# Optimization experiments

Measured on AMD Instinct MI355X. Metric: run time of the kernel, lower is better.

The kernel has to match this reference:

```python
import jax, jax.numpy as jnp
import numpy as np

B, N, E, V, D, H = 16, 4096, 524288, 4, 64, 128
MLP_IN = H + 3 + 2  # node feats + conditioning coords + two temperature scalars
SRC_T, TGT_T = 300.0, 600.0
SCALE_RANGE = 0.5


def _w(k, shape):
    return (jax.random.normal(k, shape, jnp.float32) / np.sqrt(shape[0])).astype(jnp.float32)


def setup_inputs() -> dict:
    key = jax.random.key(0)
    ks = jax.random.split(key, 32)
    inp = {
        "coordinates": jax.random.normal(ks[0], (B, N, 3), jnp.float32),
        "atom_types": jax.random.randint(ks[1], (B, N), 0, V, jnp.int32),
        "adj_list": jax.random.randint(ks[2], (E, 2), 0, N, jnp.int32),
        "edge_batch_idx": jax.random.randint(ks[3], (E,), 0, B, jnp.int32),
        "masked_elements": jnp.zeros((B, N), bool),
        # message-passing GNN params
        "embed": jax.random.normal(ks[4], (V, D), jnp.float32),
        "W_in": _w(ks[5], (D + 3, H)), "b_in": jnp.zeros(H, jnp.float32),
        "W_msg0": _w(ks[6], (2 * H, H)), "b_msg0": jnp.zeros(H, jnp.float32),
        "W_upd0": _w(ks[7], (2 * H, H)), "b_upd0": jnp.zeros(H, jnp.float32),
        "W_msg1": _w(ks[8], (2 * H, H)), "b_msg1": jnp.zeros(H, jnp.float32),
        "W_upd1": _w(ks[9], (2 * H, H)), "b_upd1": jnp.zeros(H, jnp.float32),
        "W_out": _w(ks[10], (H, H)), "b_out": jnp.zeros(H, jnp.float32),
        # scale MLP (random small weights instead of zero init so output is non-trivial)
        "Ws0": _w(ks[11], (MLP_IN, H)), "bs0": jnp.zeros(H, jnp.float32),
        "Ws1": _w(ks[12], (H, H)), "bs1": jnp.zeros(H, jnp.float32),
        "Ws2": _w(ks[13], (H, H // 2)), "bs2": jnp.zeros(H // 2, jnp.float32),
        "Ws3": _w(ks[14], (H // 2, 3)) * 0.1, "bs3": jnp.zeros(3, jnp.float32),
        # shift MLP
        "Wt0": _w(ks[15], (MLP_IN, H)), "bt0": jnp.zeros(H, jnp.float32),
        "Wt1": _w(ks[16], (H, H)), "bt1": jnp.zeros(H, jnp.float32),
        "Wt2": _w(ks[17], (H, H // 2)), "bt2": jnp.zeros(H // 2, jnp.float32),
        "Wt3": _w(ks[18], (H // 2, 3)) * 0.1, "bt3": jnp.zeros(3, jnp.float32),
    }
    return inp


def _mlp(x, layers):
    for Wl, bl in layers[:-1]:
        x = jax.nn.relu(x @ Wl + bl)
    Wl, bl = layers[-1]
    return x @ Wl + bl


def reference(coordinates, atom_types, adj_list, edge_batch_idx, masked_elements,
              embed, W_in, b_in, W_msg0, b_msg0, W_upd0, b_upd0,
              W_msg1, b_msg1, W_upd1, b_upd1, W_out, b_out,
              Ws0, bs0, Ws1, bs1, Ws2, bs2, Ws3, bs3,
              Wt0, bt0, Wt1, bt1, Wt2, bt2, Wt3, bt3):
    Bn, Nn, _ = coordinates.shape
    valid = ~masked_elements                              # [B,N]
    vf = valid[..., None].astype(coordinates.dtype)
    # ---- message passing GNN ----
    h = jnp.concatenate([embed[atom_types], coordinates], -1)  # [B,N,D+3]
    h = jax.nn.relu(h @ W_in + b_in) * vf
    hf = h.reshape(Bn * Nn, -1)
    src = edge_batch_idx * Nn + adj_list[:, 0]
    dst = edge_batch_idx * Nn + adj_list[:, 1]
    for Wm, bm, Wu, bu in ((W_msg0, b_msg0, W_upd0, b_upd0),
                           (W_msg1, b_msg1, W_upd1, b_upd1)):
        m = jax.nn.relu(jnp.concatenate([hf[src], hf[dst]], -1) @ Wm + bm)  # [E,H]
        agg = jax.ops.segment_sum(m, dst, num_segments=Bn * Nn)             # [B*N,H]
        hf = jax.nn.relu(jnp.concatenate([hf, agg], -1) @ Wu + bu)
    node_feats = (hf @ W_out + b_out).reshape(Bn, Nn, -1) * vf              # [B,N,H]
    # ---- coupling transform (phase=0: atoms with type>0 are transformed) ----
    coupling = (atom_types > 0) & valid                  # [B,N]
    cond = coordinates * (~coupling)[..., None].astype(coordinates.dtype)
    temps = jnp.broadcast_to(jnp.asarray([SRC_T, TGT_T], coordinates.dtype), (Bn, Nn, 2))
    x = jnp.concatenate([node_feats, cond, temps], -1)   # [B,N,H+5]
    raw_scales = _mlp(x, [(Ws0, bs0), (Ws1, bs1), (Ws2, bs2), (Ws3, bs3)])
    shifts = _mlp(x, [(Wt0, bt0), (Wt1, bt1), (Wt2, bt2), (Wt3, bt3)])
    m3 = coupling[..., None].astype(coordinates.dtype)   # [B,N,1]
    log_scales = jnp.tanh(raw_scales) * SCALE_RANGE * m3 * vf
    shifts = shifts * m3
    log_det = log_scales.sum((1, 2))                     # [B]
    out = jnp.exp(log_scales) * coordinates + shifts
    out = jnp.where(coupling[..., None], out, coordinates)
    return out, log_det
```

## Files before the change

kernel.cpp:

```cpp
#include <hip/hip_runtime.h>

#define NB    16
#define NN    4096
#define NNODE (NB*NN)
#define NE    524288

typedef __attribute__((ext_vector_type(8))) short bf16x8_t;
typedef __attribute__((ext_vector_type(4))) float f32x4_t;

__device__ __forceinline__ unsigned short f2bf(float f) {
    union { float f; unsigned u; } v; v.f = f;
    return (unsigned short)((v.u + 0x7FFFu + ((v.u >> 16) & 1u)) >> 16);
}
__device__ __forceinline__ float bf2f(unsigned short h) {
    union { unsigned u; float f; } v; v.u = ((unsigned)h) << 16;
    return v.f;
}

__device__ __forceinline__ void gld16(const void* g, void* l) {
    __builtin_amdgcn_global_load_lds(
        (const __attribute__((address_space(1))) unsigned int*)g,
        (__attribute__((address_space(3))) unsigned int*)l, 16, 0, 0);
}

__global__ void deg_k(const int* __restrict__ adj, const int* __restrict__ ebi, int* __restrict__ deg)
{
    int e = blockIdx.x * 256 + threadIdx.x;
    atomicAdd(&deg[ebi[e] * NN + adj[2 * e + 1]], 1);
}

__global__ void scan_k(const int* __restrict__ deg, int* __restrict__ offs)
{
    __shared__ int sums[1024];
    int t = threadIdx.x;
    int base = t * 64;
    int s = 0;
    for (int i = 0; i < 64; ++i) s += deg[base + i];
    sums[t] = s;
    __syncthreads();
    for (int off = 1; off < 1024; off <<= 1) {
        int add = (t >= off) ? sums[t - off] : 0;
        __syncthreads();
        sums[t] += add;
        __syncthreads();
    }
    int run = (t > 0) ? sums[t - 1] : 0;
    for (int i = 0; i < 64; ++i) { offs[base + i] = run; run += deg[base + i]; }
    if (t == 1023) offs[NNODE] = run;
}

__global__ void scat_k(const int* __restrict__ adj, const int* __restrict__ ebi,
                       const int* __restrict__ offs, int* __restrict__ cur, int* __restrict__ esrc)
{
    int e = blockIdx.x * 256 + threadIdx.x;
    int bb = ebi[e];
    int d = bb * NN + adj[2 * e + 1];
    int s = bb * NN + adj[2 * e + 0];
    esrc[offs[d] + atomicAdd(&cur[d], 1)] = s;
}

__global__ void prep_k(const float* __restrict__ Wm0, const float* __restrict__ Wm1,
                       const float* __restrict__ Wu0, const float* __restrict__ Wu1,
                       const float* __restrict__ Wout,
                       const float* __restrict__ Ws0, const float* __restrict__ Wt0,
                       const float* __restrict__ Ws1, const float* __restrict__ Wt1,
                       const float* __restrict__ Ws2, const float* __restrict__ Wt2,
                       const float* __restrict__ bs0, const float* __restrict__ bt0,
                       const float* __restrict__ bs1, const float* __restrict__ bt1,
                       const float* __restrict__ bs2, const float* __restrict__ bt2,
                       const float* __restrict__ bm0, const float* __restrict__ bm1,
                       unsigned short* __restrict__ Btm0, unsigned short* __restrict__ Btm1,
                       unsigned short* __restrict__ Btu0, unsigned short* __restrict__ Btu1,
                       unsigned short* __restrict__ WoutP,
                       unsigned short* __restrict__ Bt0cat, unsigned short* __restrict__ Bt1cat,
                       unsigned short* __restrict__ Bt2cat,
                       float* __restrict__ b0cat, float* __restrict__ b1cat,
                       float* __restrict__ b2cat,
                       float* __restrict__ bm0cat, float* __restrict__ bm1cat)
{
    int bid = blockIdx.x, tx = threadIdx.x;
    if (bid < 256) {
        const float* W = bid < 128 ? Wm0 : Wm1;
        unsigned short* Bt = bid < 128 ? Btm0 : Btm1;
        int idx = (bid & 127) * 256 + tx;
        int n = idx >> 7, k = idx & 127;
        float v = (n < 128) ? W[k * 128 + n] : W[(128 + k) * 128 + (n - 128)];
        Bt[n * 128 + k] = f2bf(v);
    } else if (bid < 512) {
        const float* W = bid < 384 ? Wu0 : Wu1;
        unsigned short* Bt = bid < 384 ? Btu0 : Btu1;
        int idx = ((bid - 256) & 127) * 256 + tx;
        int n = idx >> 8, k = idx & 255;
        Bt[n * 256 + k] = f2bf(W[k * 128 + n]);
    } else if (bid < 576) {
        int idx = (bid - 512) * 256 + tx;
        int n = idx >> 7, k = idx & 127;
        WoutP[n * 128 + k] = f2bf(Wout[k * 128 + n]);
    } else if (bid < 768) {
        int idx = (bid - 576) * 256 + tx;
        int n = idx / 192, kk = idx % 192;
        const float* W = n < 128 ? Ws0 : Wt0;
        int nn = n & 127;
        Bt0cat[n * 192 + kk] = f2bf(kk < 133 ? W[kk * 128 + nn] : 0.f);
    } else if (bid < 896) {
        int idx = (bid - 768) * 256 + tx;
        int n = idx >> 7, k = idx & 127;
        const float* W = n < 128 ? Ws1 : Wt1;
        Bt1cat[n * 128 + k] = f2bf(W[k * 128 + (n & 127)]);
    } else if (bid < 1024) {
        int idx = (bid - 896) * 256 + tx;
        int n = idx >> 7, k = idx & 127;
        const float* W = n < 128 ? Ws2 : Wt2;
        int nn = n & 127;
        Bt2cat[n * 128 + k] = f2bf(nn < 64 ? W[k * 64 + nn] : 0.f);
    } else if (bid == 1024) {
        b0cat[tx] = (tx < 128) ? bs0[tx] : bt0[tx - 128];
    } else if (bid == 1025) {
        b1cat[tx] = (tx < 128) ? bs1[tx] : bt1[tx - 128];
    } else if (bid == 1026) {
        int nn = tx & 127;
        b2cat[tx] = (nn < 64) ? ((tx < 128) ? bs2[nn] : bt2[nn]) : 0.f;
    } else if (bid == 1027) {
        bm0cat[tx] = (tx < 128) ? 0.f : bm0[tx - 128];
    } else {
        bm1cat[tx] = (tx < 128) ? 0.f : bm1[tx - 128];
    }
}

__device__ __forceinline__ void msg_phase(const char* act, char* Bs,
    const unsigned short* __restrict__ Bt, const float* __restrict__ bias,
    unsigned short* __restrict__ P12, size_t row0, int tx)
{
    const int wid = tx >> 6, l = tx & 63;
    const int wr = wid >> 1, wc = wid & 1;
    const int rsel = l & 15, kq = l >> 4;
    const int rg = l >> 4, cc = l & 15;
#pragma unroll
    for (int nh = 0; nh < 2; ++nh) {
        f32x4_t acc[2][4];
#pragma unroll
        for (int i = 0; i < 2; ++i)
#pragma unroll
            for (int j = 0; j < 4; ++j) { f32x4_t z = {0.f,0.f,0.f,0.f}; acc[i][j] = z; }
#pragma unroll
        for (int kc = 0; kc < 128; kc += 64) {
            __syncthreads();
#pragma unroll
            for (int p = 0; p < 4; ++p) {
                int idx = tx + p * 256;
                int n = idx >> 3, kg = idx & 7;
                int kgs = kg ^ (n & 7);
                gld16(Bt + (size_t)(nh * 128 + n) * 128 + kc + kgs * 8, Bs + idx * 16);
            }
            __syncthreads();
#pragma unroll
            for (int ks = 0; ks < 2; ++ks) {
                bf16x8_t af[2], bv[4];
#pragma unroll
                for (int fm = 0; fm < 2; ++fm) {
                    int r = wr * 32 + fm * 16 + rsel;
                    af[fm] = *(const bf16x8_t*)(act + r * 256 + kc * 2 + ((ks * 64 + kq * 16) ^ ((r & 7) << 4)));
                }
#pragma unroll
                for (int fn = 0; fn < 4; ++fn) {
                    int n = wc * 64 + fn * 16 + rsel;
                    bv[fn] = *(const bf16x8_t*)(Bs + n * 128 + ((ks * 64 + kq * 16) ^ ((n & 7) << 4)));
                }
#pragma unroll
                for (int fm = 0; fm < 2; ++fm)
#pragma unroll
                    for (int fn = 0; fn < 4; ++fn)
                        acc[fm][fn] = __builtin_amdgcn_mfma_f32_16x16x32_bf16(af[fm], bv[fn], acc[fm][fn], 0, 0, 0);
            }
        }
        __syncthreads();
#pragma unroll
        for (int fm = 0; fm < 2; ++fm)
#pragma unroll
            for (int rr = 0; rr < 4; ++rr) {
                int row = wr * 32 + fm * 16 + rg * 4 + rr;
#pragma unroll
                for (int fn = 0; fn < 4; ++fn) {
                    int col = wc * 64 + fn * 16 + cc;
                    float v = acc[fm][fn][rr] + bias[nh * 128 + col];
                    int cb = col * 2;
                    *(unsigned short*)(Bs + row * 256 + (cb & ~127) + ((cb & 127) ^ ((row & 7) << 4))) = f2bf(v);
                }
            }
        __syncthreads();
#pragma unroll
        for (int p = 0; p < 4; ++p) {
            int idx = tx + p * 256;
            int row = idx >> 4, g = idx & 15;
            int pb = g * 16;
            uint4 v = *(const uint4*)(Bs + row * 256 + (pb & ~127) + ((pb & 127) ^ ((row & 7) << 4)));
            *(uint4*)(P12 + (row0 + row) * 256 + nh * 128 + g * 8) = v;
        }
    }
}

__launch_bounds__(256, 4)
__global__ void fused_im_k(const int* __restrict__ types, const float* __restrict__ coords,
                           const unsigned char* __restrict__ maskb,
                           const float* __restrict__ embed, const float* __restrict__ W_in,
                           const float* __restrict__ b_in,
                           const unsigned short* __restrict__ Btm, const float* __restrict__ bmcat,
                           unsigned short* __restrict__ hf, unsigned short* __restrict__ P12)
{
    __shared__ __align__(16) char act[16384];
    __shared__ __align__(16) char Bs[16384];
    const int tx = threadIdx.x;
    const size_t row0 = (size_t)blockIdx.x * 64;

    float* wf = (float*)Bs;
    float* xs = (float*)(Bs + 4096);
#pragma unroll
    for (int p = 0; p < 4; ++p) {
        int idx = tx + p * 256;
        int k = idx >> 7, c = idx & 127;
        wf[idx] = (k < 7) ? W_in[k * 128 + c] : b_in[c];
    }
    if (tx < 64) {
        size_t node = row0 + tx;
        int tp = types[node];
#pragma unroll
        for (int j = 0; j < 4; ++j) xs[tx * 8 + j] = embed[(size_t)tp * 4 + j];
#pragma unroll
        for (int j = 0; j < 3; ++j) xs[tx * 8 + 4 + j] = coords[node * 3 + j];
    }
    __syncthreads();
    {
        int row = tx >> 2, c0 = (tx & 3) * 32;
        float x0 = xs[row*8+0], x1 = xs[row*8+1], x2 = xs[row*8+2], x3 = xs[row*8+3];
        float x4 = xs[row*8+4], x5 = xs[row*8+5], x6 = xs[row*8+6];
        bool msk = maskb[row0 + row];
        int swz = (row & 7) << 4;
#pragma unroll
        for (int c = 0; c < 32; ++c) {
            int col = c0 + c;
            float a = wf[7*128+col] + x0*wf[col] + x1*wf[128+col] + x2*wf[256+col]
                    + x3*wf[384+col] + x4*wf[512+col] + x5*wf[640+col] + x6*wf[768+col];
            a = msk ? 0.f : fmaxf(a, 0.f);
            int cb = col * 2;
            *(unsigned short*)(act + row * 256 + (cb & ~127) + ((cb & 127) ^ swz)) = f2bf(a);
        }
    }
    __syncthreads();
#pragma unroll
    for (int p = 0; p < 4; ++p) {
        int idx = tx + p * 256;
        int row = idx >> 4, g = idx & 15;
        int pb = g * 16;
        uint4 v = *(const uint4*)(act + row * 256 + (pb & ~127) + ((pb & 127) ^ ((row & 7) << 4)));
        *(uint4*)(hf + (row0 + row) * 128 + g * 8) = v;
    }
    msg_phase(act, Bs, Btm, bmcat, P12, row0, tx);
}

__launch_bounds__(256, 4)
__global__ void fused_um_k(const unsigned short* __restrict__ hfin,
                           const unsigned short* __restrict__ aggp,
                           const unsigned short* __restrict__ Btu, const float* __restrict__ bu,
                           const unsigned short* __restrict__ Btm, const float* __restrict__ bmcat,
                           unsigned short* __restrict__ hfout, unsigned short* __restrict__ P12)
{
    __shared__ __align__(16) char act[16384];
    __shared__ __align__(16) char Bs[16384];
    const int tx = threadIdx.x;
    const int wid = tx >> 6, l = tx & 63;
    const int wr = wid >> 1, wc = wid & 1;
    const int rsel = l & 15, kq = l >> 4, rg = l >> 4, cc = l & 15;
    const size_t row0 = (size_t)blockIdx.x * 64;

    f32x4_t acc[2][4];
#pragma unroll
    for (int i = 0; i < 2; ++i)
#pragma unroll
        for (int j = 0; j < 4; ++j) { f32x4_t z = {0.f,0.f,0.f,0.f}; acc[i][j] = z; }
#pragma unroll
    for (int kc = 0; kc < 256; kc += 64) {
        const unsigned short* Ap = (kc < 128) ? hfin : aggp;
        int kloc = kc & 127;
        __syncthreads();
#pragma unroll
        for (int p = 0; p < 4; ++p) {
            int idx = tx + p * 256;
            int n = idx >> 3, kg = idx & 7;
            int kgs = kg ^ (n & 7);
            gld16(Btu + (size_t)n * 256 + kc + kgs * 8, Bs + idx * 16);
        }
        __syncthreads();
#pragma unroll
        for (int ks = 0; ks < 2; ++ks) {
            bf16x8_t af[2], bv[4];
#pragma unroll
            for (int fm = 0; fm < 2; ++fm) {
                size_t r = row0 + wr * 32 + fm * 16 + rsel;
                af[fm] = *(const bf16x8_t*)(Ap + r * 128 + kloc + ks * 32 + kq * 8);
            }
#pragma unroll
            for (int fn = 0; fn < 4; ++fn) {
                int n = wc * 64 + fn * 16 + rsel;
                bv[fn] = *(const bf16x8_t*)(Bs + n * 128 + ((ks * 64 + kq * 16) ^ ((n & 7) << 4)));
            }
#pragma unroll
            for (int fm = 0; fm < 2; ++fm)
#pragma unroll
                for (int fn = 0; fn < 4; ++fn)
                    acc[fm][fn] = __builtin_amdgcn_mfma_f32_16x16x32_bf16(af[fm], bv[fn], acc[fm][fn], 0, 0, 0);
        }
    }
#pragma unroll
    for (int fm = 0; fm < 2; ++fm)
#pragma unroll
        for (int rr = 0; rr < 4; ++rr) {
            int row = wr * 32 + fm * 16 + rg * 4 + rr;
#pragma unroll
            for (int fn = 0; fn < 4; ++fn) {
                int col = wc * 64 + fn * 16 + cc;
                float v = fmaxf(acc[fm][fn][rr] + bu[col], 0.f);
                int cb = col * 2;
                *(unsigned short*)(act + row * 256 + (cb & ~127) + ((cb & 127) ^ ((row & 7) << 4))) = f2bf(v);
            }
        }
    __syncthreads();
#pragma unroll
    for (int p = 0; p < 4; ++p) {
        int idx = tx + p * 256;
        int row = idx >> 4, g = idx & 15;
        int pb = g * 16;
        uint4 v = *(const uint4*)(act + row * 256 + (pb & ~127) + ((pb & 127) ^ ((row & 7) << 4)));
        *(uint4*)(hfout + (row0 + row) * 128 + g * 8) = v;
    }
    msg_phase(act, Bs, Btm, bmcat, P12, row0, tx);
}

__global__ void agg_k(const unsigned short* __restrict__ P12,
                      const int* __restrict__ offs, const int* __restrict__ esrc,
                      unsigned short* __restrict__ agg)
{
    int bid = blockIdx.x;
    int chunk = gridDim.x >> 3;
    int swz = (bid & 7) * chunk + (bid >> 3);
    int node = swz * 8 + (threadIdx.x >> 5);
    int l = threadIdx.x & 31;
    int beg = offs[node], end = offs[node + 1];
    uint2 p2w = *(const uint2*)(P12 + (size_t)node * 256 + 128 + 4 * l);
    float p2a = bf2f((unsigned short)(p2w.x & 0xFFFF));
    float p2b = bf2f((unsigned short)(p2w.x >> 16));
    float p2c = bf2f((unsigned short)(p2w.y & 0xFFFF));
    float p2d = bf2f((unsigned short)(p2w.y >> 16));
    float aa = 0.f, ab = 0.f, ac = 0.f, ad = 0.f;
    int i = beg;
    for (; i + 3 < end; i += 4) {
        int s0 = esrc[i], s1 = esrc[i+1], s2 = esrc[i+2], s3 = esrc[i+3];
        uint2 v0 = *(const uint2*)(P12 + (size_t)s0 * 256 + 4 * l);
        uint2 v1 = *(const uint2*)(P12 + (size_t)s1 * 256 + 4 * l);
        uint2 v2 = *(const uint2*)(P12 + (size_t)s2 * 256 + 4 * l);
        uint2 v3 = *(const uint2*)(P12 + (size_t)s3 * 256 + 4 * l);
        aa += fmaxf(bf2f((unsigned short)(v0.x & 0xFFFF)) + p2a, 0.f);
        ab += fmaxf(bf2f((unsigned short)(v0.x >> 16))    + p2b, 0.f);
        ac += fmaxf(bf2f((unsigned short)(v0.y & 0xFFFF)) + p2c, 0.f);
        ad += fmaxf(bf2f((unsigned short)(v0.y >> 16))    + p2d, 0.f);
        aa += fmaxf(bf2f((unsigned short)(v1.x & 0xFFFF)) + p2a, 0.f);
        ab += fmaxf(bf2f((unsigned short)(v1.x >> 16))    + p2b, 0.f);
        ac += fmaxf(bf2f((unsigned short)(v1.y & 0xFFFF)) + p2c, 0.f);
        ad += fmaxf(bf2f((unsigned short)(v1.y >> 16))    + p2d, 0.f);
        aa += fmaxf(bf2f((unsigned short)(v2.x & 0xFFFF)) + p2a, 0.f);
        ab += fmaxf(bf2f((unsigned short)(v2.x >> 16))    + p2b, 0.f);
        ac += fmaxf(bf2f((unsigned short)(v2.y & 0xFFFF)) + p2c, 0.f);
        ad += fmaxf(bf2f((unsigned short)(v2.y >> 16))    + p2d, 0.f);
        aa += fmaxf(bf2f((unsigned short)(v3.x & 0xFFFF)) + p2a, 0.f);
        ab += fmaxf(bf2f((unsigned short)(v3.x >> 16))    + p2b, 0.f);
        ac += fmaxf(bf2f((unsigned short)(v3.y & 0xFFFF)) + p2c, 0.f);
        ad += fmaxf(bf2f((unsigned short)(v3.y >> 16))    + p2d, 0.f);
    }
    for (; i < end; ++i) {
        int s0 = esrc[i];
        uint2 v0 = *(const uint2*)(P12 + (size_t)s0 * 256 + 4 * l);
        aa += fmaxf(bf2f((unsigned short)(v0.x & 0xFFFF)) + p2a, 0.f);
        ab += fmaxf(bf2f((unsigned short)(v0.x >> 16))    + p2b, 0.f);
        ac += fmaxf(bf2f((unsigned short)(v0.y & 0xFFFF)) + p2c, 0.f);
        ad += fmaxf(bf2f((unsigned short)(v0.y >> 16))    + p2d, 0.f);
    }
    uint2 o;
    o.x = (unsigned)f2bf(aa) | ((unsigned)f2bf(ab) << 16);
    o.y = (unsigned)f2bf(ac) | ((unsigned)f2bf(ad) << 16);
    *(uint2*)(agg + (size_t)node * 128 + 4 * l) = o;
}

__launch_bounds__(256, 2)
__global__ void fused_ut_k(const unsigned short* __restrict__ hfin,
                           const unsigned short* __restrict__ aggp,
                           const unsigned short* __restrict__ Btu, const float* __restrict__ bu,
                           const unsigned short* __restrict__ WoutP, const float* __restrict__ bOut,
                           const unsigned short* __restrict__ Bt0, const float* __restrict__ b0,
                           const unsigned short* __restrict__ Bt1, const float* __restrict__ b1,
                           const unsigned short* __restrict__ Bt2, const float* __restrict__ b2,
                           const float* __restrict__ Ws3, const float* __restrict__ bs3,
                           const float* __restrict__ Wt3, const float* __restrict__ bt3,
                           const float* __restrict__ coords, const int* __restrict__ types,
                           const unsigned char* __restrict__ maskb,
                           float* __restrict__ outc, float* __restrict__ partial)
{
    __shared__ __align__(16) char act[32768];
    __shared__ __align__(16) char hfn[16384];
    __shared__ __align__(16) char Bs[32768];
    const int tx = threadIdx.x;
    const int wid = tx >> 6, l = tx & 63;
    const int rsel = l & 15, kq = l >> 4, rg = l >> 4, cc = l & 15;
    const size_t row0 = (size_t)blockIdx.x * 64;
    const int wr = wid >> 1, wc = wid & 1;

    {
        f32x4_t acc[2][4];
#pragma unroll
        for (int i = 0; i < 2; ++i)
#pragma unroll
            for (int j = 0; j < 4; ++j) { f32x4_t z = {0.f,0.f,0.f,0.f}; acc[i][j] = z; }
#pragma unroll
        for (int kc = 0; kc < 256; kc += 64) {
            const unsigned short* Ap = (kc < 128) ? hfin : aggp;
            int kloc = kc & 127;
            __syncthreads();
#pragma unroll
            for (int p = 0; p < 4; ++p) {
                int idx = tx + p * 256;
                int n = idx >> 3, kg = idx & 7;
                int kgs = kg ^ (n & 7);
                gld16(Btu + (size_t)n * 256 + kc + kgs * 8, Bs + idx * 16);
            }
            __syncthreads();
#pragma unroll
            for (int ks = 0; ks < 2; ++ks) {
                bf16x8_t af[2], bv[4];
#pragma unroll
                for (int fm = 0; fm < 2; ++fm) {
                    size_t r = row0 + wr * 32 + fm * 16 + rsel;
                    af[fm] = *(const bf16x8_t*)(Ap + r * 128 + kloc + ks * 32 + kq * 8);
                }
#pragma unroll
                for (int fn = 0; fn < 4; ++fn) {
                    int n = wc * 64 + fn * 16 + rsel;
                    bv[fn] = *(const bf16x8_t*)(Bs + n * 128 + ((ks * 64 + kq * 16) ^ ((n & 7) << 4)));
                }
#pragma unroll
                for (int fm = 0; fm < 2; ++fm)
#pragma unroll
                    for (int fn = 0; fn < 4; ++fn)
                        acc[fm][fn] = __builtin_amdgcn_mfma_f32_16x16x32_bf16(af[fm], bv[fn], acc[fm][fn], 0, 0, 0);
            }
        }
#pragma unroll
        for (int fm = 0; fm < 2; ++fm)
#pragma unroll
            for (int rr = 0; rr < 4; ++rr) {
                int row = wr * 32 + fm * 16 + rg * 4 + rr;
#pragma unroll
                for (int fn = 0; fn < 4; ++fn) {
                    int col = wc * 64 + fn * 16 + cc;
                    float v = fmaxf(acc[fm][fn][rr] + bu[col], 0.f);
                    int cb = col * 2;
                    *(unsigned short*)(hfn + row * 256 + (cb & ~127) + ((cb & 127) ^ ((row & 7) << 4))) = f2bf(v);
                }
            }
    }
    __syncthreads();

    {
        f32x4_t acc[2][4];
#pragma unroll
        for (int i = 0; i < 2; ++i)
#pragma unroll
            for (int j = 0; j < 4; ++j) { f32x4_t z = {0.f,0.f,0.f,0.f}; acc[i][j] = z; }
#pragma unroll
        for (int kc = 0; kc < 128; kc += 64) {
            __syncthreads();
#pragma unroll
            for (int p = 0; p < 4; ++p) {
                int idx = tx + p * 256;
                int n = idx >> 3, kg = idx & 7;
                int kgs = kg ^ (n & 7);
                gld16(WoutP + (size_t)n * 128 + kc + kgs * 8, Bs + idx * 16);
            }
            __syncthreads();
#pragma unroll
            for (int ks = 0; ks < 2; ++ks) {
                bf16x8_t af[2], bv[4];
#pragma unroll
                for (int fm = 0; fm < 2; ++fm) {
                    int r = wr * 32 + fm * 16 + rsel;
                    af[fm] = *(const bf16x8_t*)(hfn + r * 256 + kc * 2 + ((ks * 64 + kq * 16) ^ ((r & 7) << 4)));
                }
#pragma unroll
                for (int fn = 0; fn < 4; ++fn) {
                    int n = wc * 64 + fn * 16 + rsel;
                    bv[fn] = *(const bf16x8_t*)(Bs + n * 128 + ((ks * 64 + kq * 16) ^ ((n & 7) << 4)));
                }
#pragma unroll
                for (int fm = 0; fm < 2; ++fm)
#pragma unroll
                    for (int fn = 0; fn < 4; ++fn)
                        acc[fm][fn] = __builtin_amdgcn_mfma_f32_16x16x32_bf16(af[fm], bv[fn], acc[fm][fn], 0, 0, 0);
            }
        }
#pragma unroll
        for (int fm = 0; fm < 2; ++fm)
#pragma unroll
            for (int rr = 0; rr < 4; ++rr) {
                int row = wr * 32 + fm * 16 + rg * 4 + rr;
                bool zero = maskb[row0 + row];
#pragma unroll
                for (int fn = 0; fn < 4; ++fn) {
                    int col = wc * 64 + fn * 16 + cc;
                    float v = acc[fm][fn][rr] + bOut[col];
                    if (zero) v = 0.f;
                    int cb = col * 2;
                    *(unsigned short*)(act + row * 512 + (cb & ~127) + ((cb & 127) ^ ((row & 7) << 4))) = f2bf(v);
                }
            }
    }
#pragma unroll
    for (int p = 0; p < 16; ++p) {
        int idx = tx + p * 256;
        int row = idx >> 6, ci = idx & 63;
        int col = 128 + ci;
        size_t node = row0 + row;
        bool coup = (types[node] > 0) && !maskb[node];
        float v;
        if (ci < 3)       v = coup ? 0.f : coords[node * 3 + ci];
        else if (ci == 3) v = 300.f;
        else if (ci == 4) v = 600.f;
        else              v = 0.f;
        int cb = col * 2;
        *(unsigned short*)(act + row * 512 + (cb & ~127) + ((cb & 127) ^ ((row & 7) << 4))) = f2bf(v);
    }
    __syncthreads();

#pragma unroll
    for (int layer = 0; layer < 3; ++layer) {
        const unsigned short* Bt = layer == 0 ? Bt0 : (layer == 1 ? Bt1 : Bt2);
        const float* bb = layer == 0 ? b0 : (layer == 1 ? b1 : b2);
        const int ldbt = layer == 0 ? 192 : 128;
        const int Ktot = layer == 0 ? 192 : 128;
        const int kbase = (layer == 0) ? 0 : (wc ? 256 : 0);
        f32x4_t acc[2][8];
#pragma unroll
        for (int i = 0; i < 2; ++i)
#pragma unroll
            for (int j = 0; j < 8; ++j) { f32x4_t z = {0.f,0.f,0.f,0.f}; acc[i][j] = z; }
        for (int kc = 0; kc < Ktot; kc += 64) {
            __syncthreads();
#pragma unroll
            for (int p = 0; p < 8; ++p) {
                int idx = tx + p * 256;
                int n = idx >> 3, kg = idx & 7;
                int kgs = kg ^ (n & 7);
                gld16(Bt + (size_t)n * ldbt + kc + kgs * 8, Bs + idx * 16);
            }
            __syncthreads();
#pragma unroll
            for (int ks = 0; ks < 2; ++ks) {
                bf16x8_t af[2], bv[8];
#pragma unroll
                for (int fm = 0; fm < 2; ++fm) {
                    int r = wr * 32 + fm * 16 + rsel;
                    af[fm] = *(const bf16x8_t*)(act + r * 512 + kbase + kc * 2 + ((ks * 64 + kq * 16) ^ ((r & 7) << 4)));
                }
#pragma unroll
                for (int fn = 0; fn < 8; ++fn) {
                    int n = wc * 128 + fn * 16 + rsel;
                    bv[fn] = *(const bf16x8_t*)(Bs + n * 128 + ((ks * 64 + kq * 16) ^ ((n & 7) << 4)));
                }
#pragma unroll
                for (int fm = 0; fm < 2; ++fm)
#pragma unroll
                    for (int fn = 0; fn < 8; ++fn)
                        acc[fm][fn] = __builtin_amdgcn_mfma_f32_16x16x32_bf16(af[fm], bv[fn], acc[fm][fn], 0, 0, 0);
            }
        }
        __syncthreads();
#pragma unroll
        for (int fm = 0; fm < 2; ++fm)
#pragma unroll
            for (int rr = 0; rr < 4; ++rr) {
                int row = wr * 32 + fm * 16 + rg * 4 + rr;
#pragma unroll
                for (int fn = 0; fn < 8; ++fn) {
                    int col = wc * 128 + fn * 16 + cc;
                    float v = fmaxf(acc[fm][fn][rr] + bb[col], 0.f);
                    int cb = col * 2;
                    *(unsigned short*)(act + row * 512 + (cb & ~127) + ((cb & 127) ^ ((row & 7) << 4))) = f2bf(v);
                }
            }
        __syncthreads();
    }

    float* W3f = (float*)hfn;
    float* red = (float*)(hfn + 2048);
    for (int i = tx; i < 384; i += 256)
        W3f[i] = (i < 192) ? Ws3[i] : Wt3[i - 192];
    __syncthreads();
    {
        int row = tx >> 2, sub = tx & 3;
        int swz = (row & 7) << 4;
        float rs0 = 0.f, rs1 = 0.f, rs2 = 0.f, sh0 = 0.f, sh1 = 0.f, sh2 = 0.f;
#pragma unroll
        for (int kk = 0; kk < 16; ++kk) {
            int k = sub * 16 + kk;
            float av = bf2f(*(const unsigned short*)(act + row * 512 + ((k * 2) ^ swz)));
            float bv = bf2f(*(const unsigned short*)(act + row * 512 + 256 + ((k * 2) ^ swz)));
            rs0 += av * W3f[k * 3 + 0]; rs1 += av * W3f[k * 3 + 1]; rs2 += av * W3f[k * 3 + 2];
            sh0 += bv * W3f[192 + k * 3 + 0]; sh1 += bv * W3f[192 + k * 3 + 1]; sh2 += bv * W3f[192 + k * 3 + 2];
        }
        rs0 += __shfl_xor(rs0, 1); rs0 += __shfl_xor(rs0, 2);
        rs1 += __shfl_xor(rs1, 1); rs1 += __shfl_xor(rs1, 2);
        rs2 += __shfl_xor(rs2, 1); rs2 += __shfl_xor(rs2, 2);
        sh0 += __shfl_xor(sh0, 1); sh0 += __shfl_xor(sh0, 2);
        sh1 += __shfl_xor(sh1, 1); sh1 += __shfl_xor(sh1, 2);
        sh2 += __shfl_xor(sh2, 1); sh2 += __shfl_xor(sh2, 2);
        if (sub == 0) {
            size_t node = row0 + row;
            bool coup = (types[node] > 0) && !maskb[node];
            float c0 = coords[node * 3 + 0], c1 = coords[node * 3 + 1], c2 = coords[node * 3 + 2];
            float ls0 = 0.f, ls1 = 0.f, ls2 = 0.f, o0 = c0, o1 = c1, o2 = c2;
            if (coup) {
                ls0 = tanhf(rs0 + bs3[0]) * 0.5f;
                ls1 = tanhf(rs1 + bs3[1]) * 0.5f;
                ls2 = tanhf(rs2 + bs3[2]) * 0.5f;
                o0 = expf(ls0) * c0 + sh0 + bt3[0];
                o1 = expf(ls1) * c1 + sh1 + bt3[1];
                o2 = expf(ls2) * c2 + sh2 + bt3[2];
            }
            outc[node * 3 + 0] = o0;
            outc[node * 3 + 1] = o1;
            outc[node * 3 + 2] = o2;
            red[row] = ls0 + ls1 + ls2;
        }
    }
    __syncthreads();
    for (int s = 32; s > 0; s >>= 1) {
        if (tx < s) red[tx] += red[tx + s];
        __syncthreads();
    }
    if (tx == 0) partial[blockIdx.x] = red[0];
}

__global__ void red_k(const float* __restrict__ partial, float* __restrict__ ldet)
{
    __shared__ float s[1024];
    int t = threadIdx.x;
#pragma unroll
    for (int p = 0; p < 4; ++p) s[t + p * 256] = partial[t + p * 256];
    __syncthreads();
    if (t < 16) {
        float v = 0.f;
        for (int i = 0; i < 64; ++i) v += s[t * 64 + i];
        ldet[t] = v;
    }
}

extern "C" void kernel_launch(void* const* d_in, const int* in_sizes, int n_in,
                              void* d_out, int out_size, void* d_ws, size_t ws_size,
                              hipStream_t stream)
{
    (void)in_sizes; (void)n_in; (void)out_size; (void)ws_size;
    const float* coords = (const float*)d_in[0];
    const int*   types  = (const int*)d_in[1];
    const int*   adj    = (const int*)d_in[2];
    const int*   ebi    = (const int*)d_in[3];
    const unsigned char* maskb = (const unsigned char*)d_in[4];
    const float* embed  = (const float*)d_in[5];
    const float* W_in   = (const float*)d_in[6];
    const float* b_in   = (const float*)d_in[7];
    const float* W_msg[2] = {(const float*)d_in[8],  (const float*)d_in[12]};
    const float* b_msg[2] = {(const float*)d_in[9],  (const float*)d_in[13]};
    const float* W_upd[2] = {(const float*)d_in[10], (const float*)d_in[14]};
    const float* b_upd[2] = {(const float*)d_in[11], (const float*)d_in[15]};
    const float* W_out = (const float*)d_in[16]; const float* b_out = (const float*)d_in[17];
    const float* Ws0 = (const float*)d_in[18]; const float* bs0 = (const float*)d_in[19];
    const float* Ws1 = (const float*)d_in[20]; const float* bs1 = (const float*)d_in[21];
    const float* Ws2 = (const float*)d_in[22]; const float* bs2 = (const float*)d_in[23];
    const float* Ws3 = (const float*)d_in[24]; const float* bs3 = (const float*)d_in[25];
    const float* Wt0 = (const float*)d_in[26]; const float* bt0 = (const float*)d_in[27];
    const float* Wt1 = (const float*)d_in[28]; const float* bt1 = (const float*)d_in[29];
    const float* Wt2 = (const float*)d_in[30]; const float* bt2 = (const float*)d_in[31];
    const float* Wt3 = (const float*)d_in[32]; const float* bt3 = (const float*)d_in[33];

    char* ws = (char*)d_ws;
    size_t off = 0;
    auto alloc = [&](size_t bytes) { void* p = ws + off; off += (bytes + 255) & ~(size_t)255; return p; };
    unsigned short* hf   = (unsigned short*)alloc((size_t)NNODE * 128 * 2);
    unsigned short* P12  = (unsigned short*)alloc((size_t)NNODE * 256 * 2);
    unsigned short* agg  = (unsigned short*)alloc((size_t)NNODE * 128 * 2);
    int*   deg  = (int*)alloc((size_t)NNODE * 4);
    int*   offs = (int*)alloc((size_t)(NNODE + 1) * 4);
    int*   cur  = (int*)alloc((size_t)NNODE * 4);
    int*   esrc = (int*)alloc((size_t)NE * 4);
    unsigned short* Btm0 = (unsigned short*)alloc(256 * 128 * 2);
    unsigned short* Btm1 = (unsigned short*)alloc(256 * 128 * 2);
    unsigned short* Btu0 = (unsigned short*)alloc(128 * 256 * 2);
    unsigned short* Btu1 = (unsigned short*)alloc(128 * 256 * 2);
    unsigned short* WoutP  = (unsigned short*)alloc(128 * 128 * 2);
    unsigned short* Bt0cat = (unsigned short*)alloc(256 * 192 * 2);
    unsigned short* Bt1cat = (unsigned short*)alloc(256 * 128 * 2);
    unsigned short* Bt2cat = (unsigned short*)alloc(256 * 128 * 2);
    float* b0cat  = (float*)alloc(256 * 4);
    float* b1cat  = (float*)alloc(256 * 4);
    float* b2cat  = (float*)alloc(256 * 4);
    float* bm0cat = (float*)alloc(256 * 4);
    float* bm1cat = (float*)alloc(256 * 4);
    float* partial = (float*)alloc(1024 * 4);

    hipMemsetAsync(deg, 0, (size_t)NNODE * 4, stream);
    hipMemsetAsync(cur, 0, (size_t)NNODE * 4, stream);

    deg_k<<<NE / 256, 256, 0, stream>>>(adj, ebi, deg);
    scan_k<<<1, 1024, 0, stream>>>(deg, offs);
    scat_k<<<NE / 256, 256, 0, stream>>>(adj, ebi, offs, cur, esrc);
    prep_k<<<1029, 256, 0, stream>>>(W_msg[0], W_msg[1], W_upd[0], W_upd[1], W_out,
                                     Ws0, Wt0, Ws1, Wt1, Ws2, Wt2,
                                     bs0, bt0, bs1, bt1, bs2, bt2, b_msg[0], b_msg[1],
                                     Btm0, Btm1, Btu0, Btu1, WoutP,
                                     Bt0cat, Bt1cat, Bt2cat,
                                     b0cat, b1cat, b2cat, bm0cat, bm1cat);

    fused_im_k<<<1024, 256, 0, stream>>>(types, coords, maskb, embed, W_in, b_in,
                                         Btm0, bm0cat, hf, P12);
    agg_k<<<NNODE / 8, 256, 0, stream>>>(P12, offs, esrc, agg);
    fused_um_k<<<1024, 256, 0, stream>>>(hf, agg, Btu0, b_upd[0], Btm1, bm1cat, hf, P12);
    agg_k<<<NNODE / 8, 256, 0, stream>>>(P12, offs, esrc, agg);

    float* outc = (float*)d_out;
    fused_ut_k<<<1024, 256, 0, stream>>>(hf, agg, Btu1, b_upd[1], WoutP, b_out,
                                         Bt0cat, b0cat, Bt1cat, b1cat, Bt2cat, b2cat,
                                         Ws3, bs3, Wt3, bt3,
                                         coords, types, maskb, outc, partial);
    red_k<<<1, 256, 0, stream>>>(partial, outc + (size_t)NNODE * 3);
}
```

Measured before the change: 246.4 us.

## Widen aggregation gathers, fold memsets into prep kernel, swizzle GEMM tile order

The aggregation kernel now gives each node 16 lanes that each load 16 bytes (8 bf16) per edge, where before it used 32 lanes loading 8 bytes. This halves the number of gather instructions and doubles the per-node accumulation work per thread. The two memsets for the degree and cursor arrays are replaced by extra blocks in the weight-prep kernel, removing two separate operations. The three fused GEMM kernels also remap block index to row tile with an 8-way swizzle so that adjacent blocks are spread across tiles, presumably to balance XCD/L2 locality.

Result: faster. 234.9 us (-4.7%).

```diff
diff --git a/kernel.cpp b/kernel.cpp
--- a/kernel.cpp
+++ b/kernel.cpp
@@ -76,7 +76,8 @@
                        unsigned short* __restrict__ Bt2cat,
                        float* __restrict__ b0cat, float* __restrict__ b1cat,
                        float* __restrict__ b2cat,
-                       float* __restrict__ bm0cat, float* __restrict__ bm1cat)
+                       float* __restrict__ bm0cat, float* __restrict__ bm1cat,
+                       int* __restrict__ deg, int* __restrict__ cur)
 {
     int bid = blockIdx.x, tx = threadIdx.x;
     if (bid < 256) {
@@ -122,8 +123,13 @@
         b2cat[tx] = (nn < 64) ? ((tx < 128) ? bs2[nn] : bt2[nn]) : 0.f;
     } else if (bid == 1027) {
         bm0cat[tx] = (tx < 128) ? 0.f : bm0[tx - 128];
+    } else if (bid == 1028) {
+        bm1cat[tx] = (tx < 128) ? 0.f : bm1[tx - 128];
     } else {
-        bm1cat[tx] = (tx < 128) ? 0.f : bm1[tx - 128];
+        int idx = (bid - 1029) * 256 + tx;
+        int4 z = {0, 0, 0, 0};
+        if (idx < 16384) ((int4*)deg)[idx] = z;
+        else             ((int4*)cur)[idx - 16384] = z;
     }
 }
 
@@ -210,7 +216,8 @@
     __shared__ __align__(16) char act[16384];
     __shared__ __align__(16) char Bs[16384];
     const int tx = threadIdx.x;
-    const size_t row0 = (size_t)blockIdx.x * 64;
+    const int tile = ((blockIdx.x & 7) * (gridDim.x >> 3)) + (blockIdx.x >> 3);
+    const size_t row0 = (size_t)tile * 64;
 
     float* wf = (float*)Bs;
     float* xs = (float*)(Bs + 4096);
@@ -270,7 +277,8 @@
     const int wid = tx >> 6, l = tx & 63;
     const int wr = wid >> 1, wc = wid & 1;
     const int rsel = l & 15, kq = l >> 4, rg = l >> 4, cc = l & 15;
-    const size_t row0 = (size_t)blockIdx.x * 64;
+    const int tile = ((blockIdx.x & 7) * (gridDim.x >> 3)) + (blockIdx.x >> 3);
+    const size_t row0 = (size_t)tile * 64;
 
     f32x4_t acc[2][4];
 #pragma unroll
@@ -342,51 +350,50 @@
     int bid = blockIdx.x;
     int chunk = gridDim.x >> 3;
     int swz = (bid & 7) * chunk + (bid >> 3);
-    int node = swz * 8 + (threadIdx.x >> 5);
-    int l = threadIdx.x & 31;
+    int node = swz * 16 + (threadIdx.x >> 4);
+    int l = threadIdx.x & 15;
     int beg = offs[node], end = offs[node + 1];
-    uint2 p2w = *(const uint2*)(P12 + (size_t)node * 256 + 128 + 4 * l);
-    float p2a = bf2f((unsigned short)(p2w.x & 0xFFFF));
-    float p2b = bf2f((unsigned short)(p2w.x >> 16));
-    float p2c = bf2f((unsigned short)(p2w.y & 0xFFFF));
-    float p2d = bf2f((unsigned short)(p2w.y >> 16));
-    float aa = 0.f, ab = 0.f, ac = 0.f, ad = 0.f;
+    float p2c[8], ac[8];
+    {
+        uint4 w = *(const uint4*)(P12 + (size_t)node * 256 + 128 + 8 * l);
+        unsigned ww[4] = {w.x, w.y, w.z, w.w};
+#pragma unroll
+        for (int j = 0; j < 4; ++j) {
+            p2c[2*j]   = bf2f((unsigned short)(ww[j] & 0xFFFF));
+            p2c[2*j+1] = bf2f((unsigned short)(ww[j] >> 16));
+        }
+    }
+#pragma unroll
+    for (int j = 0; j < 8; ++j) ac[j] = 0.f;
+
+    auto accum = [&](uint4 v) {
+        unsigned ww[4] = {v.x, v.y, v.z, v.w};
+#pragma unroll
+        for (int j = 0; j < 4; ++j) {
+            ac[2*j]   += fmaxf(bf2f((unsigned short)(ww[j] & 0xFFFF)) + p2c[2*j],   0.f);
+            ac[2*j+1] += fmaxf(bf2f((unsigned short)(ww[j] >> 16))    + p2c[2*j+1], 0.f);
+        }
+    };
+
     int i = beg;
     for (; i + 3 < end; i += 4) {
         int s0 = esrc[i], s1 = esrc[i+1], s2 = esrc[i+2], s3 = esrc[i+3];
-        uint2 v0 = *(const uint2*)(P12 + (size_t)s0 * 256 + 4 * l);
-        uint2 v1 = *(const uint2*)(P12 + (size_t)s1 * 256 + 4 * l);
-        uint2 v2 = *(const uint2*)(P12 + (size_t)s2 * 256 + 4 * l);
-        uint2 v3 = *(const uint2*)(P12 + (size_t)s3 * 256 + 4 * l);
-        aa += fmaxf(bf2f((unsigned short)(v0.x & 0xFFFF)) + p2a, 0.f);
-        ab += fmaxf(bf2f((unsigned short)(v0.x >> 16))    + p2b, 0.f);
-        ac += fmaxf(bf2f((unsigned short)(v0.y & 0xFFFF)) + p2c, 0.f);
-        ad += fmaxf(bf2f((unsigned short)(v0.y >> 16))    + p2d, 0.f);
-        aa += fmaxf(bf2f((unsigned short)(v1.x & 0xFFFF)) + p2a, 0.f);
-        ab += fmaxf(bf2f((unsigned short)(v1.x >> 16))    + p2b, 0.f);
-        ac += fmaxf(bf2f((unsigned short)(v1.y & 0xFFFF)) + p2c, 0.f);
-        ad += fmaxf(bf2f((unsigned short)(v1.y >> 16))    + p2d, 0.f);
-        aa += fmaxf(bf2f((unsigned short)(v2.x & 0xFFFF)) + p2a, 0.f);
-        ab += fmaxf(bf2f((unsigned short)(v2.x >> 16))    + p2b, 0.f);
-        ac += fmaxf(bf2f((unsigned short)(v2.y & 0xFFFF)) + p2c, 0.f);
-        ad += fmaxf(bf2f((unsigned short)(v2.y >> 16))    + p2d, 0.f);
-        aa += fmaxf(bf2f((unsigned short)(v3.x & 0xFFFF)) + p2a, 0.f);
-        ab += fmaxf(bf2f((unsigned short)(v3.x >> 16))    + p2b, 0.f);
-        ac += fmaxf(bf2f((unsigned short)(v3.y & 0xFFFF)) + p2c, 0.f);
-        ad += fmaxf(bf2f((unsigned short)(v3.y >> 16))    + p2d, 0.f);
+        uint4 v0 = *(const uint4*)(P12 + (size_t)s0 * 256 + 8 * l);
+        uint4 v1 = *(const uint4*)(P12 + (size_t)s1 * 256 + 8 * l);
+        uint4 v2 = *(const uint4*)(P12 + (size_t)s2 * 256 + 8 * l);
+        uint4 v3 = *(const uint4*)(P12 + (size_t)s3 * 256 + 8 * l);
+        accum(v0); accum(v1); accum(v2); accum(v3);
     }
     for (; i < end; ++i) {
-        int s0 = esrc[i];
-        uint2 v0 = *(const uint2*)(P12 + (size_t)s0 * 256 + 4 * l);
-        aa += fmaxf(bf2f((unsigned short)(v0.x & 0xFFFF)) + p2a, 0.f);
-        ab += fmaxf(bf2f((unsigned short)(v0.x >> 16))    + p2b, 0.f);
-        ac += fmaxf(bf2f((unsigned short)(v0.y & 0xFFFF)) + p2c, 0.f);
-        ad += fmaxf(bf2f((unsigned short)(v0.y >> 16))    + p2d, 0.f);
-    }
-    uint2 o;
-    o.x = (unsigned)f2bf(aa) | ((unsigned)f2bf(ab) << 16);
-    o.y = (unsigned)f2bf(ac) | ((unsigned)f2bf(ad) << 16);
-    *(uint2*)(agg + (size_t)node * 128 + 4 * l) = o;
+        uint4 v0 = *(const uint4*)(P12 + (size_t)esrc[i] * 256 + 8 * l);
+        accum(v0);
+    }
+    uint4 o;
+    o.x = (unsigned)f2bf(ac[0]) | ((unsigned)f2bf(ac[1]) << 16);
+    o.y = (unsigned)f2bf(ac[2]) | ((unsigned)f2bf(ac[3]) << 16);
+    o.z = (unsigned)f2bf(ac[4]) | ((unsigned)f2bf(ac[5]) << 16);
+    o.w = (unsigned)f2bf(ac[6]) | ((unsigned)f2bf(ac[7]) << 16);
+    *(uint4*)(agg + (size_t)node * 128 + 8 * l) = o;
 }
 
 __launch_bounds__(256, 2)
@@ -409,7 +416,8 @@
     const int tx = threadIdx.x;
     const int wid = tx >> 6, l = tx & 63;
     const int rsel = l & 15, kq = l >> 4, rg = l >> 4, cc = l & 15;
-    const size_t row0 = (size_t)blockIdx.x * 64;
+    const int tile = ((blockIdx.x & 7) * (gridDim.x >> 3)) + (blockIdx.x >> 3);
+    const size_t row0 = (size_t)tile * 64;
     const int wr = wid >> 1, wc = wid & 1;
 
     {
@@ -643,7 +651,7 @@
         if (tx < s) red[tx] += red[tx + s];
         __syncthreads();
     }
-    if (tx == 0) partial[blockIdx.x] = red[0];
+    if (tx == 0) partial[tile] = red[0];
 }
 
 __global__ void red_k(const float* __restrict__ partial, float* __restrict__ ldet)
@@ -712,24 +720,21 @@
     float* bm1cat = (float*)alloc(256 * 4);
     float* partial = (float*)alloc(1024 * 4);
 
-    hipMemsetAsync(deg, 0, (size_t)NNODE * 4, stream);
-    hipMemsetAsync(cur, 0, (size_t)NNODE * 4, stream);
-
-    deg_k<<<NE / 256, 256, 0, stream>>>(adj, ebi, deg);
-    scan_k<<<1, 1024, 0, stream>>>(deg, offs);
-    scat_k<<<NE / 256, 256, 0, stream>>>(adj, ebi, offs, cur, esrc);
-    prep_k<<<1029, 256, 0, stream>>>(W_msg[0], W_msg[1], W_upd[0], W_upd[1], W_out,
+    prep_k<<<1157, 256, 0, stream>>>(W_msg[0], W_msg[1], W_upd[0], W_upd[1], W_out,
                                      Ws0, Wt0, Ws1, Wt1, Ws2, Wt2,
                                      bs0, bt0, bs1, bt1, bs2, bt2, b_msg[0], b_msg[1],
                                      Btm0, Btm1, Btu0, Btu1, WoutP,
                                      Bt0cat, Bt1cat, Bt2cat,
-                                     b0cat, b1cat, b2cat, bm0cat, bm1cat);
+                                     b0cat, b1cat, b2cat, bm0cat, bm1cat, deg, cur);
+    deg_k<<<NE / 256, 256, 0, stream>>>(adj, ebi, deg);
+    scan_k<<<1, 1024, 0, stream>>>(deg, offs);
+    scat_k<<<NE / 256, 256, 0, stream>>>(adj, ebi, offs, cur, esrc);
 
     fused_im_k<<<1024, 256, 0, stream>>>(types, coords, maskb, embed, W_in, b_in,
                                          Btm0, bm0cat, hf, P12);
-    agg_k<<<NNODE / 8, 256, 0, stream>>>(P12, offs, esrc, agg);
+    agg_k<<<NNODE / 16, 256, 0, stream>>>(P12, offs, esrc, agg);
     fused_um_k<<<1024, 256, 0, stream>>>(hf, agg, Btu0, b_upd[0], Btm1, bm1cat, hf, P12);
-    agg_k<<<NNODE / 8, 256, 0, stream>>>(P12, offs, esrc, agg);
+    agg_k<<<NNODE / 16, 256, 0, stream>>>(P12, offs, esrc, agg);
 
     float* outc = (float*)d_out;
     fused_ut_k<<<1024, 256, 0, stream>>>(hf, agg, Btu1, b_upd[1], WoutP, b_out,
```
